# Performance work log

Measured on AMD Instinct MI355X. Metric: run time of the kernel, lower is better.

## Reference

```python
import jax, jax.numpy as jnp
import numpy as np

N = 50000      # nodes
E = 800000     # edges
IN_DIM = 256
HID = 96
OUT = 64
K = 2
ALPHA = 0.15
SCALING = 1.8  # NormalizedGCNConv scaling_factor
EPS = 1e-12    # torch F.normalize eps


def setup_inputs() -> dict:
    key = jax.random.key(0)
    ks = jax.random.split(key, 8)
    x = jax.random.normal(ks[0], (N, IN_DIM), jnp.float32)
    edge_index = jax.random.randint(ks[1], (2, E), 0, N, dtype=jnp.int64)
    def lin(k, fi, fo):
        s = 1.0 / np.sqrt(fi)
        kw, kb = jax.random.split(k)
        W = jax.random.uniform(kw, (fi, fo), jnp.float32, -s, s)
        b = jax.random.uniform(kb, (fo,), jnp.float32, -s, s)
        return W, b
    W0, b0 = lin(ks[2], IN_DIM, HID)   # convs[0]
    W1, b1 = lin(ks[3], HID, HID)      # convs[1]
    Wx, bx = lin(ks[4], HID, OUT)      # convx
    return {"x": x, "edge_index": edge_index,
            "W0": W0, "b0": b0, "W1": W1, "b1": b1, "Wx": Wx, "bx": bx}


def _l2norm(x):
    n = jnp.linalg.norm(x, axis=1, keepdims=True)
    return x / jnp.maximum(n, EPS)


def _gcn_norm(edge_index):
    # add self loops, symmetric normalization D^-1/2 (A+I) D^-1/2
    loop = jnp.arange(N, dtype=edge_index.dtype)
    row = jnp.concatenate([edge_index[0], loop])
    col = jnp.concatenate([edge_index[1], loop])
    deg = jax.ops.segment_sum(jnp.ones(row.shape[0], jnp.float32), col, num_segments=N)
    dinv = jnp.where(deg > 0, jax.lax.rsqrt(jnp.maximum(deg, 1.0)), 0.0)
    norm = dinv[row] * dinv[col]   # [E+N]
    return row, col, norm


def _norm_gcn_conv(x, W, b, row, col, norm):
    # linear -> L2 normalize * 1.8 -> APPNP(K, alpha), eval mode (no dropout)
    x = x @ W + b
    x = _l2norm(x) * SCALING
    h = x
    for _ in range(K):
        agg = jax.ops.segment_sum(x[row] * norm[:, None], col, num_segments=N)
        x = (1.0 - ALPHA) * agg + ALPHA * h
    return x


def reference(x, edge_index, W0, b0, W1, b1, Wx, bx):
    row, col, norm = _gcn_norm(edge_index)
    out = jax.nn.relu(_norm_gcn_conv(x, W0, b0, row, col, norm))
    # depth=3, link_len=2: loop runs i=1 only, residual condition never fires
    out = _l2norm(_norm_gcn_conv(out, W1, b1, row, col, norm)) * 1.5
    return _norm_gcn_conv(out, Wx, bx, row, col, norm)
```

## Files before the change

kernel.cpp:

```cpp
#include <hip/hip_runtime.h>
#include <hip/hip_fp16.h>
#include <math.h>

#define BETA_C 0.85f
#define ALF_C  0.15f
#define SLOTS 48
#define SCALE_Q 16.0f
#define INV_SQ  0.0625f

typedef _Float16 f16x8 __attribute__((ext_vector_type(8)));
typedef float f32x4 __attribute__((ext_vector_type(4)));
typedef float f32x2 __attribute__((ext_vector_type(2)));
typedef int i32x4 __attribute__((ext_vector_type(4)));

__device__ inline f16x8 as_h8(uint4 v) { union { uint4 u; f16x8 h; } U; U.u = v; return U.h; }

__device__ inline void unpack8(uint4 v, float* f) {
    union { uint4 u; _Float16 h[8]; } U; U.u = v;
#pragma unroll
    for (int i = 0; i < 8; ++i) f[i] = (float)U.h[i];
}

__device__ inline void acc_q(uint2 q, float* acc) {
    f32x2 f0 = __builtin_amdgcn_cvt_pk_f32_fp8((int)q.x, false);
    f32x2 f1 = __builtin_amdgcn_cvt_pk_f32_fp8((int)q.x, true);
    f32x2 f2 = __builtin_amdgcn_cvt_pk_f32_fp8((int)q.y, false);
    f32x2 f3 = __builtin_amdgcn_cvt_pk_f32_fp8((int)q.y, true);
    acc[0] += f0.x; acc[1] += f0.y; acc[2] += f1.x; acc[3] += f1.y;
    acc[4] += f2.x; acc[5] += f2.y; acc[6] += f3.x; acc[7] += f3.y;
}
__device__ inline uint2 pack_q(const float* r) {
    int lo = __builtin_amdgcn_cvt_pk_fp8_f32(r[0] * SCALE_Q, r[1] * SCALE_Q, 0, false);
    lo = __builtin_amdgcn_cvt_pk_fp8_f32(r[2] * SCALE_Q, r[3] * SCALE_Q, lo, true);
    int hi = __builtin_amdgcn_cvt_pk_fp8_f32(r[4] * SCALE_Q, r[5] * SCALE_Q, 0, false);
    hi = __builtin_amdgcn_cvt_pk_fp8_f32(r[6] * SCALE_Q, r[7] * SCALE_Q, hi, true);
    return make_uint2((unsigned)lo, (unsigned)hi);
}

__global__ __launch_bounds__(256) void k_fill_tlp(
        const int* __restrict__ row, const int* __restrict__ col,
        int* __restrict__ cur, int* __restrict__ adj, int E, unsigned mulc) {
    int cls = blockIdx.x & 7;
    int e = (blockIdx.x >> 3) * 256 + threadIdx.x;
    if (e >= E) return;
    int c = __builtin_nontemporal_load(col + e);
    if ((int)(((unsigned long long)(unsigned)c * mulc) >> 32) != cls) return;
    int r = __builtin_nontemporal_load(row + e);
    int p = atomicAdd(&cur[c], 1);
    if (p < SLOTS) adj[(size_t)c * SLOTS + p] = r;
}

__global__ void k_prep(const int* __restrict__ cur, float2* __restrict__ dinv2,
                       int* __restrict__ adj, int n, int t0,
                       const float* __restrict__ W0, const float* __restrict__ W1,
                       const float* __restrict__ Wx, ushort* __restrict__ WT0,
                       ushort* __restrict__ WT1, ushort* __restrict__ WTx) {
    int idx = blockIdx.x * blockDim.x + threadIdx.x;
    if (idx < n) {
        int deg = cur[idx];
        float degf = (float)deg + 1.0f;
        dinv2[idx] = make_float2(rsqrtf(degf), ALF_C * sqrtf(degf));
        int ds = min(deg, SLOTS);
        int d4 = (ds + 3) & ~3;
        int* ap = adj + (size_t)idx * SLOTS;
        for (int p = ds; p < d4; ++p) ap[p] = idx;
    } else if (idx >= t0) {
        const int S0 = 96 * 256, S1 = 96 * 96, S2 = 64 * 96;
        int li = idx - t0;
        const float* W; ushort* WT; int FI, FO;
        if (li < S0)           { W = W0; WT = WT0; FI = 256; FO = 96; }
        else if (li < S0 + S1) { W = W1; WT = WT1; FI = 96;  FO = 96; li -= S0; }
        else if (li < S0+S1+S2){ W = Wx; WT = WTx; FI = 96;  FO = 64; li -= S0 + S1; }
        else return;
        int nrow = li / FI, k = li % FI;
        _Float16 hv = (_Float16)W[(size_t)k * FO + nrow];
        WT[li] = *(ushort*)&hv;
    }
}

template<int FI, int FO, int ASRC_F16, int WQ>
__global__ __launch_bounds__(256) void k_gemm_mfma(
        const void* __restrict__ Xv, const ushort* __restrict__ WT,
        const float* __restrict__ Bias, const float2* __restrict__ dinv2,
        ushort* __restrict__ H, unsigned char* __restrict__ Hq,
        int n, float scale) {
    constexpr int NT = FO / 16;
    constexpr int CPR = FI / 8;
    __shared__ ushort sA[64 * FI];
    __shared__ ushort sW[FO * FI];
    const int tid = threadIdx.x;
    const int rb = blockIdx.x * 64;

    {
        constexpr int TOT = FO * CPR;
#pragma unroll
        for (int idx = tid; idx < TOT; idx += 256) {
            int nrow = idx / CPR, c = idx % CPR;
            uint4 v = *(((const uint4*)WT) + (size_t)nrow * CPR + c);
            int byte = ((nrow * FI + c * 8) * 2) ^ ((nrow & 7) << 4);
            *(uint4*)((char*)sW + byte) = v;
        }
    }
    {
        constexpr int TOT = 64 * CPR;
#pragma unroll
        for (int idx = tid; idx < TOT; idx += 256) {
            int r = idx / CPR, c = idx % CPR;
            int gr = rb + r;
            uint4 v = make_uint4(0u, 0u, 0u, 0u);
            if (ASRC_F16) {
                if (gr < n) v = *(((const uint4*)Xv) + (size_t)gr * CPR + c);
            } else {
                if (gr < n) {
                    const float4* Xp = (const float4*)Xv;
                    float4 f0 = Xp[(size_t)gr * (FI / 4) + c * 2];
                    float4 f1 = Xp[(size_t)gr * (FI / 4) + c * 2 + 1];
                    _Float16 hv[8] = {(_Float16)f0.x, (_Float16)f0.y, (_Float16)f0.z,
                                      (_Float16)f0.w, (_Float16)f1.x, (_Float16)f1.y,
                                      (_Float16)f1.z, (_Float16)f1.w};
                    v = *(uint4*)hv;
                }
            }
            int byte = ((r * FI + c * 8) * 2) ^ ((r & 7) << 4);
            *(uint4*)((char*)sA + byte) = v;
        }
    }
    __syncthreads();

    const int lane = tid & 63;
    const int wave = tid >> 6;
    const int lcol = lane & 15;
    const int lk = lane >> 4;

    f32x4 acc[NT];
#pragma unroll
    for (int t = 0; t < NT; ++t) acc[t] = (f32x4){0.f, 0.f, 0.f, 0.f};

    const int arow = wave * 16 + lcol;
    char* sAb = (char*)sA;
    char* sWb = (char*)sW;
#pragma unroll
    for (int s = 0; s < FI / 32; ++s) {
        int abyte = ((arow * FI + s * 32 + lk * 8) * 2) ^ ((arow & 7) << 4);
        f16x8 af = *(f16x8*)(sAb + abyte);
#pragma unroll
        for (int t = 0; t < NT; ++t) {
            int nrow = t * 16 + lcol;
            int bbyte = ((nrow * FI + s * 32 + lk * 8) * 2) ^ ((nrow & 7) << 4);
            f16x8 bf = *(f16x8*)(sWb + bbyte);
            acc[t] = __builtin_amdgcn_mfma_f32_16x16x32_f16(af, bf, acc[t], 0, 0, 0);
        }
    }

    float bv[NT];
#pragma unroll
    for (int t = 0; t < NT; ++t) bv[t] = Bias[t * 16 + lcol];
    float ss[4] = {0.f, 0.f, 0.f, 0.f};
#pragma unroll
    for (int t = 0; t < NT; ++t)
#pragma unroll
        for (int r = 0; r < 4; ++r) {
            acc[t][r] += bv[t];
            ss[r] += acc[t][r] * acc[t][r];
        }
    for (int m = 1; m < 16; m <<= 1) {
#pragma unroll
        for (int r = 0; r < 4; ++r) ss[r] += __shfl_xor(ss[r], m, 64);
    }
#pragma unroll
    for (int r = 0; r < 4; ++r) {
        int grow = rb + wave * 16 + lk * 4 + r;
        if (grow < n) {
            float sc = scale * dinv2[grow].x / fmaxf(sqrtf(ss[r]), 1e-12f);
#pragma unroll
            for (int t = 0; t < NT; ++t) {
                float v = acc[t][r] * sc;
                _Float16 hv = (_Float16)v;
                H[(size_t)grow * FO + t * 16 + lcol] = *(ushort*)&hv;
                if (WQ) {
                    float vs = v * SCALE_Q;
                    int b = __builtin_amdgcn_cvt_pk_fp8_f32(vs, vs, 0, false);
                    Hq[(size_t)grow * FO + t * 16 + lcol] = (unsigned char)(b & 0xff);
                }
            }
        }
    }
}

template<int C8>
__device__ inline void gather_q(const unsigned char* __restrict__ tq,
                                const int* __restrict__ ap,
                                int d4, int j, float* acc) {
    const size_t RB = C8 * 8;
    const int jb = j * 8;
    int e = 0;
    for (; e + 8 <= d4; e += 8) {
        i32x4 a0 = __builtin_nontemporal_load((const i32x4*)ap + (e >> 2));
        i32x4 a1 = __builtin_nontemporal_load((const i32x4*)ap + (e >> 2) + 1);
        uint2 q0 = *(const uint2*)(tq + (size_t)(unsigned)a0[0] * RB + jb);
        uint2 q1 = *(const uint2*)(tq + (size_t)(unsigned)a0[1] * RB + jb);
        uint2 q2 = *(const uint2*)(tq + (size_t)(unsigned)a0[2] * RB + jb);
        uint2 q3 = *(const uint2*)(tq + (size_t)(unsigned)a0[3] * RB + jb);
        uint2 q4 = *(const uint2*)(tq + (size_t)(unsigned)a1[0] * RB + jb);
        uint2 q5 = *(const uint2*)(tq + (size_t)(unsigned)a1[1] * RB + jb);
        uint2 q6 = *(const uint2*)(tq + (size_t)(unsigned)a1[2] * RB + jb);
        uint2 q7 = *(const uint2*)(tq + (size_t)(unsigned)a1[3] * RB + jb);
        acc_q(q0, acc); acc_q(q1, acc); acc_q(q2, acc); acc_q(q3, acc);
        acc_q(q4, acc); acc_q(q5, acc); acc_q(q6, acc); acc_q(q7, acc);
    }
    if (e < d4) {
        i32x4 a0 = __builtin_nontemporal_load((const i32x4*)ap + (e >> 2));
        uint2 q0 = *(const uint2*)(tq + (size_t)(unsigned)a0[0] * RB + jb);
        uint2 q1 = *(const uint2*)(tq + (size_t)(unsigned)a0[1] * RB + jb);
        uint2 q2 = *(const uint2*)(tq + (size_t)(unsigned)a0[2] * RB + jb);
        uint2 q3 = *(const uint2*)(tq + (size_t)(unsigned)a0[3] * RB + jb);
        acc_q(q0, acc); acc_q(q1, acc); acc_q(q2, acc); acc_q(q3, acc);
    }
}

template<int C8>
__device__ inline void gather_h(const uint4* __restrict__ tab,
                                const int* __restrict__ ap,
                                int d4, int j, f16x8& A0, f16x8& A1) {
    int e = 0;
    for (; e + 8 <= d4; e += 8) {
        i32x4 a0 = __builtin_nontemporal_load((const i32x4*)ap + (e >> 2));
        i32x4 a1 = __builtin_nontemporal_load((const i32x4*)ap + (e >> 2) + 1);
        uint4 v0 = tab[(size_t)(unsigned)a0[0] * C8 + j];
        uint4 v1 = tab[(size_t)(unsigned)a0[1] * C8 + j];
        uint4 v2 = tab[(size_t)(unsigned)a0[2] * C8 + j];
        uint4 v3 = tab[(size_t)(unsigned)a0[3] * C8 + j];
        uint4 v4 = tab[(size_t)(unsigned)a1[0] * C8 + j];
        uint4 v5 = tab[(size_t)(unsigned)a1[1] * C8 + j];
        uint4 v6 = tab[(size_t)(unsigned)a1[2] * C8 + j];
        uint4 v7 = tab[(size_t)(unsigned)a1[3] * C8 + j];
        A0 += (as_h8(v0) + as_h8(v1)) + (as_h8(v2) + as_h8(v3));
        A1 += (as_h8(v4) + as_h8(v5)) + (as_h8(v6) + as_h8(v7));
    }
    if (e < d4) {
        i32x4 a0 = __builtin_nontemporal_load((const i32x4*)ap + (e >> 2));
        uint4 v0 = tab[(size_t)(unsigned)a0[0] * C8 + j];
        uint4 v1 = tab[(size_t)(unsigned)a0[1] * C8 + j];
        uint4 v2 = tab[(size_t)(unsigned)a0[2] * C8 + j];
        uint4 v3 = tab[(size_t)(unsigned)a0[3] * C8 + j];
        A0 += as_h8(v0) + as_h8(v1);
        A1 += as_h8(v2) + as_h8(v3);
    }
}

template<int C8, int TPB, int QG, int WQ>
__global__ __launch_bounds__(TPB) void k_prop1(
        const uint4* __restrict__ y0h, const unsigned char* __restrict__ y0q,
        uint4* __restrict__ y1h, unsigned char* __restrict__ y1q,
        const int* __restrict__ adj, const int* __restrict__ cnt,
        const float2* __restrict__ dinv2, int n) {
    int tid = threadIdx.x;
    int j = tid % C8, cl = tid / C8;
    int c = blockIdx.x * (TPB / C8) + cl;
    if (c >= n) return;
    uint4 sv = y0h[(size_t)c * C8 + j];
    float d = dinv2[c].x;
    float a = BETA_C * d * d;
    int deg = min(cnt[c], SLOTS);
    int d4 = (deg + 3) & ~3;
    float coef_s = (a + ALF_C) - a * (float)(d4 - deg);
    float acc[8] = {0, 0, 0, 0, 0, 0, 0, 0};
    if (QG) {
        gather_q<C8>(y0q, adj + (size_t)c * SLOTS, d4, j, acc);
#pragma unroll
        for (int i = 0; i < 8; ++i) acc[i] *= INV_SQ;
    } else {
        f16x8 A0 = {0, 0, 0, 0, 0, 0, 0, 0};
        f16x8 A1 = {0, 0, 0, 0, 0, 0, 0, 0};
        gather_h<C8>(y0h, adj + (size_t)c * SLOTS, d4, j, A0, A1);
#pragma unroll
        for (int i = 0; i < 8; ++i) acc[i] = (float)A0[i] + (float)A1[i];
    }
    float sf[8];
    unpack8(sv, sf);
    float r[8];
    _Float16 hv[8];
#pragma unroll
    for (int i = 0; i < 8; ++i) {
        r[i] = a * acc[i] + coef_s * sf[i];
        hv[i] = (_Float16)r[i];
    }
    y1h[(size_t)c * C8 + j] = *(uint4*)hv;
    if (WQ) *(uint2*)(y1q + (size_t)c * (C8 * 8) + j * 8) = pack_q(r);
}

template<int C8, int TPB, int ACT, int OUTF32, int NORM, int QG>
__global__ __launch_bounds__(TPB) void k_prop2(
        const uint4* __restrict__ y1h, const unsigned char* __restrict__ y1q,
        const uint4* __restrict__ y0h, void* __restrict__ out,
        const int* __restrict__ adj, const int* __restrict__ cnt,
        const float2* __restrict__ dinv2, int n, float nscale) {
    __shared__ float ssh[NORM ? TPB : 1];
    int tid = threadIdx.x;
    int j = tid % C8, cl = tid / C8;
    int c = blockIdx.x * (TPB / C8) + cl;
    if (!NORM && c >= n) return;
    bool on = !NORM || c < n;
    float res[8] = {0, 0, 0, 0, 0, 0, 0, 0};
    if (on) {
        uint4 sv1 = y1h[(size_t)c * C8 + j];
        uint4 sv0 = y0h[(size_t)c * C8 + j];
        float2 dv = dinv2[c];
        float a = BETA_C * dv.x;
        float t = dv.y;
        int deg = min(cnt[c], SLOTS);
        int d4 = (deg + 3) & ~3;
        float coef_s = a * (1.0f - (float)(d4 - deg));
        float acc[8] = {0, 0, 0, 0, 0, 0, 0, 0};
        if (QG) {
            gather_q<C8>(y1q, adj + (size_t)c * SLOTS, d4, j, acc);
#pragma unroll
            for (int i = 0; i < 8; ++i) acc[i] *= INV_SQ;
        } else {
            f16x8 A0 = {0, 0, 0, 0, 0, 0, 0, 0};
            f16x8 A1 = {0, 0, 0, 0, 0, 0, 0, 0};
            gather_h<C8>(y1h, adj + (size_t)c * SLOTS, d4, j, A0, A1);
#pragma unroll
            for (int i = 0; i < 8; ++i) acc[i] = (float)A0[i] + (float)A1[i];
        }
        float sf[8], tf[8];
        unpack8(sv1, sf);
        unpack8(sv0, tf);
#pragma unroll
        for (int i = 0; i < 8; ++i) {
            res[i] = a * acc[i] + coef_s * sf[i] + t * tf[i];
            if (ACT) res[i] = fmaxf(res[i], 0.f);
        }
    }
    if (NORM) {
        float part = 0.f;
#pragma unroll
        for (int i = 0; i < 8; ++i) part += res[i] * res[i];
        ssh[tid] = part;
        __syncthreads();
        if (!on) return;
        float tot = 0.f;
#pragma unroll
        for (int q = 0; q < C8; ++q) tot += ssh[cl * C8 + q];
        float sc = nscale / fmaxf(sqrtf(tot), 1e-12f);
        _Float16 hv[8];
#pragma unroll
        for (int i = 0; i < 8; ++i) hv[i] = (_Float16)(res[i] * sc);
        ((uint4*)out)[(size_t)c * C8 + j] = *(uint4*)hv;
    } else if (OUTF32) {
        float4* op = (float4*)out;
        op[(size_t)c * (C8 * 2) + j * 2]     = make_float4(res[0], res[1], res[2], res[3]);
        op[(size_t)c * (C8 * 2) + j * 2 + 1] = make_float4(res[4], res[5], res[6], res[7]);
    } else {
        _Float16 hv[8];
#pragma unroll
        for (int i = 0; i < 8; ++i) hv[i] = (_Float16)res[i];
        ((uint4*)out)[(size_t)c * C8 + j] = *(uint4*)hv;
    }
}

extern "C" void kernel_launch(void* const* d_in, const int* in_sizes, int n_in,
                              void* d_out, int out_size, void* d_ws, size_t ws_size,
                              hipStream_t stream) {
    const float* x  = (const float*)d_in[0];
    const int*   ei = (const int*)d_in[1];
    const float* W0 = (const float*)d_in[2];
    const float* b0 = (const float*)d_in[3];
    const float* W1 = (const float*)d_in[4];
    const float* b1 = (const float*)d_in[5];
    const float* Wx = (const float*)d_in[6];
    const float* bx = (const float*)d_in[7];
    float* out = (float*)d_out;

    const int N = in_sizes[0] / 256;
    const int E = in_sizes[1] / 2;
    const int* row = ei;
    const int* col = ei + E;

    char* ws = (char*)d_ws;
    size_t off = 0;
    auto alloc = [&](size_t bytes) -> char* {
        char* p = ws + off;
        off += (bytes + 255) & ~(size_t)255;
        return p;
    };
    int*    cur   = (int*)alloc((size_t)N * 4);
    float2* dinv2 = (float2*)alloc((size_t)N * 8);
    int*    adj   = (int*)alloc((size_t)N * SLOTS * 4);
    ushort* WT0   = (ushort*)alloc((size_t)96 * 256 * 2);
    ushort* WT1   = (ushort*)alloc((size_t)96 * 96 * 2);
    ushort* WTx   = (ushort*)alloc((size_t)64 * 96 * 2);
    ushort* Hh    = (ushort*)alloc((size_t)N * 96 * 2);
    ushort* T1h   = (ushort*)alloc((size_t)N * 96 * 2);
    ushort* T2h   = (ushort*)alloc((size_t)N * 96 * 2);
    unsigned char* Hq  = (unsigned char*)alloc((size_t)N * 96);
    unsigned char* T1q = (unsigned char*)alloc((size_t)N * 96);
    (void)ws_size; (void)n_in; (void)out_size;

    unsigned mulc = (unsigned)((((unsigned long long)8 << 32) + (unsigned)N - 1) / (unsigned)N);

    hipMemsetAsync(cur, 0, (size_t)N * 4, stream);
    {
        int chunks = (E + 255) / 256;
        k_fill_tlp<<<chunks * 8, 256, 0, stream>>>(row, col, cur, adj, E, mulc);
    }
    {
        int t0 = ((N + 255) / 256) * 256;
        int tot = t0 + 96 * 256 + 96 * 96 + 64 * 96;
        k_prep<<<(tot + 255) / 256, 256, 0, stream>>>(cur, dinv2, adj, N, t0,
                                                      W0, W1, Wx, WT0, WT1, WTx);
    }

    int gblk = (N + 63) / 64;
    int gp12 = (N + 15) / 16;
    int gp8  = (N + 31) / 32;

    k_gemm_mfma<256, 96, 0, 1><<<gblk, 256, 0, stream>>>(x, WT0, b0, dinv2, Hh, Hq, N, 1.8f);
    k_prop1<12, 192, 1, 1><<<gp12, 192, 0, stream>>>(
        (const uint4*)Hh, Hq, (uint4*)T1h, T1q, adj, cur, dinv2, N);
    k_prop2<12, 192, 1, 0, 0, 1><<<gp12, 192, 0, stream>>>(
        (const uint4*)T1h, T1q, (const uint4*)Hh, T2h, adj, cur, dinv2, N, 0.f);

    k_gemm_mfma<96, 96, 1, 1><<<gblk, 256, 0, stream>>>(T2h, WT1, b1, dinv2, Hh, Hq, N, 1.8f);
    k_prop1<12, 192, 1, 1><<<gp12, 192, 0, stream>>>(
        (const uint4*)Hh, Hq, (uint4*)T1h, T1q, adj, cur, dinv2, N);
    k_prop2<12, 192, 0, 0, 1, 1><<<gp12, 192, 0, stream>>>(
        (const uint4*)T1h, T1q, (const uint4*)Hh, T2h, adj, cur, dinv2, N, 1.5f);

    k_gemm_mfma<96, 64, 1, 0><<<gblk, 256, 0, stream>>>(T2h, WTx, bx, dinv2, Hh, Hq, N, 1.8f);
    k_prop1<8, 256, 0, 0><<<gp8, 256, 0, stream>>>(
        (const uint4*)Hh, Hq, (uint4*)T1h, T1q, adj, cur, dinv2, N);
    k_prop2<8, 256, 0, 1, 0, 0><<<gp8, 256, 0, stream>>>(
        (const uint4*)T1h, T1q, (const uint4*)Hh, out, adj, cur, dinv2, N, 0.f);
}
```

Measured before the change: 216.0 us.

## Widen propagation gathers to 16 fp8 per lane and vectorize edge fill

Propagation kernels now have each thread handle 16 features, gathering 16-byte fp8 rows instead of 8-byte chunks. This halves the threads per node and doubles bytes per load. The last layer also switches from fp16 gathers to fp8-quantized gathers, adding quantization error to the final output. The fill kernel reads edges four at a time with vector loads, which cuts index traffic and the number of threads.

Result: slower. 221.0 us (+2.3%).

```diff
diff --git a/kernel.cpp b/kernel.cpp
--- a/kernel.cpp
+++ b/kernel.cpp
@@ -29,6 +29,10 @@
     acc[0] += f0.x; acc[1] += f0.y; acc[2] += f1.x; acc[3] += f1.y;
     acc[4] += f2.x; acc[5] += f2.y; acc[6] += f3.x; acc[7] += f3.y;
 }
+__device__ inline void acc16(uint4 q, float* acc) {
+    acc_q(make_uint2(q.x, q.y), acc);
+    acc_q(make_uint2(q.z, q.w), acc + 8);
+}
 __device__ inline uint2 pack_q(const float* r) {
     int lo = __builtin_amdgcn_cvt_pk_fp8_f32(r[0] * SCALE_Q, r[1] * SCALE_Q, 0, false);
     lo = __builtin_amdgcn_cvt_pk_fp8_f32(r[2] * SCALE_Q, r[3] * SCALE_Q, lo, true);
@@ -37,17 +41,45 @@
     return make_uint2((unsigned)lo, (unsigned)hi);
 }
 
-__global__ __launch_bounds__(256) void k_fill_tlp(
+__global__ __launch_bounds__(256) void k_fill_q(
         const int* __restrict__ row, const int* __restrict__ col,
         int* __restrict__ cur, int* __restrict__ adj, int E, unsigned mulc) {
     int cls = blockIdx.x & 7;
-    int e = (blockIdx.x >> 3) * 256 + threadIdx.x;
+    int q = (blockIdx.x >> 3) * 256 + threadIdx.x;
+    int e = q * 4;
     if (e >= E) return;
-    int c = __builtin_nontemporal_load(col + e);
-    if ((int)(((unsigned long long)(unsigned)c * mulc) >> 32) != cls) return;
-    int r = __builtin_nontemporal_load(row + e);
-    int p = atomicAdd(&cur[c], 1);
-    if (p < SLOTS) adj[(size_t)c * SLOTS + p] = r;
+    i32x4 cv;
+    bool full = (e + 3 < E);
+    if (full) {
+        cv = __builtin_nontemporal_load((const i32x4*)col + q);
+    } else {
+#pragma unroll
+        for (int i = 0; i < 4; ++i) cv[i] = (e + i < E) ? col[e + i] : 0;
+    }
+    bool m[4]; bool any = false;
+#pragma unroll
+    for (int i = 0; i < 4; ++i) {
+        bool valid = full || (e + i < E);
+        m[i] = valid &&
+               ((int)(((unsigned long long)(unsigned)cv[i] * mulc) >> 32) == cls);
+        any |= m[i];
+    }
+    if (!any) return;
+    i32x4 rv;
+    if (full) {
+        rv = __builtin_nontemporal_load((const i32x4*)row + q);
+    } else {
+#pragma unroll
+        for (int i = 0; i < 4; ++i) rv[i] = (e + i < E) ? row[e + i] : 0;
+    }
+#pragma unroll
+    for (int i = 0; i < 4; ++i) {
+        if (m[i]) {
+            int c = cv[i];
+            int p = atomicAdd(&cur[c], 1);
+            if (p < SLOTS) adj[(size_t)c * SLOTS + p] = rv[i];
+        }
+    }
 }
 
 __global__ void k_prep(const int* __restrict__ cur, float2* __restrict__ dinv2,
@@ -78,7 +110,7 @@
     }
 }
 
-template<int FI, int FO, int ASRC_F16, int WQ>
+template<int FI, int FO, int ASRC_F16>
 __global__ __launch_bounds__(256) void k_gemm_mfma(
         const void* __restrict__ Xv, const ushort* __restrict__ WT,
         const float* __restrict__ Bias, const float2* __restrict__ dinv2,
@@ -177,185 +209,155 @@
                 float v = acc[t][r] * sc;
                 _Float16 hv = (_Float16)v;
                 H[(size_t)grow * FO + t * 16 + lcol] = *(ushort*)&hv;
-                if (WQ) {
-                    float vs = v * SCALE_Q;
-                    int b = __builtin_amdgcn_cvt_pk_fp8_f32(vs, vs, 0, false);
-                    Hq[(size_t)grow * FO + t * 16 + lcol] = (unsigned char)(b & 0xff);
-                }
+                float vs = v * SCALE_Q;
+                int b = __builtin_amdgcn_cvt_pk_fp8_f32(vs, vs, 0, false);
+                Hq[(size_t)grow * FO + t * 16 + lcol] = (unsigned char)(b & 0xff);
             }
         }
     }
 }
 
-template<int C8>
-__device__ inline void gather_q(const unsigned char* __restrict__ tq,
-                                const int* __restrict__ ap,
-                                int d4, int j, float* acc) {
-    const size_t RB = C8 * 8;
-    const int jb = j * 8;
+template<int RB>
+__device__ inline void gather_q16(const unsigned char* __restrict__ tq,
+                                  const int* __restrict__ ap,
+                                  int d4, int jb, float* acc) {
     int e = 0;
     for (; e + 8 <= d4; e += 8) {
         i32x4 a0 = __builtin_nontemporal_load((const i32x4*)ap + (e >> 2));
         i32x4 a1 = __builtin_nontemporal_load((const i32x4*)ap + (e >> 2) + 1);
-        uint2 q0 = *(const uint2*)(tq + (size_t)(unsigned)a0[0] * RB + jb);
-        uint2 q1 = *(const uint2*)(tq + (size_t)(unsigned)a0[1] * RB + jb);
-        uint2 q2 = *(const uint2*)(tq + (size_t)(unsigned)a0[2] * RB + jb);
-        uint2 q3 = *(const uint2*)(tq + (size_t)(unsigned)a0[3] * RB + jb);
-        uint2 q4 = *(const uint2*)(tq + (size_t)(unsigned)a1[0] * RB + jb);
-        uint2 q5 = *(const uint2*)(tq + (size_t)(unsigned)a1[1] * RB + jb);
-        uint2 q6 = *(const uint2*)(tq + (size_t)(unsigned)a1[2] * RB + jb);
-        uint2 q7 = *(const uint2*)(tq + (size_t)(unsigned)a1[3] * RB + jb);
-        acc_q(q0, acc); acc_q(q1, acc); acc_q(q2, acc); acc_q(q3, acc);
-        acc_q(q4, acc); acc_q(q5, acc); acc_q(q6, acc); acc_q(q7, acc);
+        uint4 v0 = *(const uint4*)(tq + (size_t)(unsigned)a0[0] * RB + jb);
+        uint4 v1 = *(const uint4*)(tq + (size_t)(unsigned)a0[1] * RB + jb);
+        uint4 v2 = *(const uint4*)(tq + (size_t)(unsigned)a0[2] * RB + jb);
+        uint4 v3 = *(const uint4*)(tq + (size_t)(unsigned)a0[3] * RB + jb);
+        uint4 v4 = *(const uint4*)(tq + (size_t)(unsigned)a1[0] * RB + jb);
+        uint4 v5 = *(const uint4*)(tq + (size_t)(unsigned)a1[1] * RB + jb);
+        uint4 v6 = *(const uint4*)(tq + (size_t)(unsigned)a1[2] * RB + jb);
+        uint4 v7 = *(const uint4*)(tq + (size_t)(unsigned)a1[3] * RB + jb);
+        acc16(v0, acc); acc16(v1, acc); acc16(v2, acc); acc16(v3, acc);
+        acc16(v4, acc); acc16(v5, acc); acc16(v6, acc); acc16(v7, acc);
     }
     if (e < d4) {
         i32x4 a0 = __builtin_nontemporal_load((const i32x4*)ap + (e >> 2));
-        uint2 q0 = *(const uint2*)(tq + (size_t)(unsigned)a0[0] * RB + jb);
-        uint2 q1 = *(const uint2*)(tq + (size_t)(unsigned)a0[1] * RB + jb);
-        uint2 q2 = *(const uint2*)(tq + (size_t)(unsigned)a0[2] * RB + jb);
-        uint2 q3 = *(const uint2*)(tq + (size_t)(unsigned)a0[3] * RB + jb);
-        acc_q(q0, acc); acc_q(q1, acc); acc_q(q2, acc); acc_q(q3, acc);
-    }
-}
-
-template<int C8>
-__device__ inline void gather_h(const uint4* __restrict__ tab,
-                                const int* __restrict__ ap,
-                                int d4, int j, f16x8& A0, f16x8& A1) {
-    int e = 0;
-    for (; e + 8 <= d4; e += 8) {
-        i32x4 a0 = __builtin_nontemporal_load((const i32x4*)ap + (e >> 2));
-        i32x4 a1 = __builtin_nontemporal_load((const i32x4*)ap + (e >> 2) + 1);
-        uint4 v0 = tab[(size_t)(unsigned)a0[0] * C8 + j];
-        uint4 v1 = tab[(size_t)(unsigned)a0[1] * C8 + j];
-        uint4 v2 = tab[(size_t)(unsigned)a0[2] * C8 + j];
-        uint4 v3 = tab[(size_t)(unsigned)a0[3] * C8 + j];
-        uint4 v4 = tab[(size_t)(unsigned)a1[0] * C8 + j];
-        uint4 v5 = tab[(size_t)(unsigned)a1[1] * C8 + j];
-        uint4 v6 = tab[(size_t)(unsigned)a1[2] * C8 + j];
-        uint4 v7 = tab[(size_t)(unsigned)a1[3] * C8 + j];
-        A0 += (as_h8(v0) + as_h8(v1)) + (as_h8(v2) + as_h8(v3));
-        A1 += (as_h8(v4) + as_h8(v5)) + (as_h8(v6) + as_h8(v7));
-    }
-    if (e < d4) {
-        i32x4 a0 = __builtin_nontemporal_load((const i32x4*)ap + (e >> 2));
-        uint4 v0 = tab[(size_t)(unsigned)a0[0] * C8 + j];
-        uint4 v1 = tab[(size_t)(unsigned)a0[1] * C8 + j];
-        uint4 v2 = tab[(size_t)(unsigned)a0[2] * C8 + j];
-        uint4 v3 = tab[(size_t)(unsigned)a0[3] * C8 + j];
-        A0 += as_h8(v0) + as_h8(v1);
-        A1 += as_h8(v2) + as_h8(v3);
-    }
-}
-
-template<int C8, int TPB, int QG, int WQ>
-__global__ __launch_bounds__(TPB) void k_prop1(
+        uint4 v0 = *(const uint4*)(tq + (size_t)(unsigned)a0[0] * RB + jb);
+        uint4 v1 = *(const uint4*)(tq + (size_t)(unsigned)a0[1] * RB + jb);
+        uint4 v2 = *(const uint4*)(tq + (size_t)(unsigned)a0[2] * RB + jb);
+        uint4 v3 = *(const uint4*)(tq + (size_t)(unsigned)a0[3] * RB + jb);
+        acc16(v0, acc); acc16(v1, acc); acc16(v2, acc); acc16(v3, acc);
+    }
+}
+
+template<int CQ, int TPB>
+__global__ __launch_bounds__(TPB) void k_prop1_q(
         const uint4* __restrict__ y0h, const unsigned char* __restrict__ y0q,
         uint4* __restrict__ y1h, unsigned char* __restrict__ y1q,
         const int* __restrict__ adj, const int* __restrict__ cnt,
         const float2* __restrict__ dinv2, int n) {
+    constexpr int C8H = CQ * 2;
+    constexpr int RB = CQ * 16;
     int tid = threadIdx.x;
-    int j = tid % C8, cl = tid / C8;
-    int c = blockIdx.x * (TPB / C8) + cl;
+    int j = tid % CQ, cl = tid / CQ;
+    int c = blockIdx.x * (TPB / CQ) + cl;
     if (c >= n) return;
-    uint4 sv = y0h[(size_t)c * C8 + j];
+    uint4 sv0 = y0h[(size_t)c * C8H + j * 2];
+    uint4 sv1 = y0h[(size_t)c * C8H + j * 2 + 1];
     float d = dinv2[c].x;
     float a = BETA_C * d * d;
     int deg = min(cnt[c], SLOTS);
     int d4 = (deg + 3) & ~3;
     float coef_s = (a + ALF_C) - a * (float)(d4 - deg);
-    float acc[8] = {0, 0, 0, 0, 0, 0, 0, 0};
-    if (QG) {
-        gather_q<C8>(y0q, adj + (size_t)c * SLOTS, d4, j, acc);
-#pragma unroll
-        for (int i = 0; i < 8; ++i) acc[i] *= INV_SQ;
-    } else {
-        f16x8 A0 = {0, 0, 0, 0, 0, 0, 0, 0};
-        f16x8 A1 = {0, 0, 0, 0, 0, 0, 0, 0};
-        gather_h<C8>(y0h, adj + (size_t)c * SLOTS, d4, j, A0, A1);
-#pragma unroll
-        for (int i = 0; i < 8; ++i) acc[i] = (float)A0[i] + (float)A1[i];
-    }
-    float sf[8];
-    unpack8(sv, sf);
-    float r[8];
-    _Float16 hv[8];
-#pragma unroll
-    for (int i = 0; i < 8; ++i) {
-        r[i] = a * acc[i] + coef_s * sf[i];
+    float aq = a * INV_SQ;
+    float acc[16];
+#pragma unroll
+    for (int i = 0; i < 16; ++i) acc[i] = 0.f;
+    gather_q16<RB>(y0q, adj + (size_t)c * SLOTS, d4, j * 16, acc);
+    float sf[16];
+    unpack8(sv0, sf);
+    unpack8(sv1, sf + 8);
+    float r[16];
+    _Float16 hv[16];
+#pragma unroll
+    for (int i = 0; i < 16; ++i) {
+        r[i] = aq * acc[i] + coef_s * sf[i];
         hv[i] = (_Float16)r[i];
     }
-    y1h[(size_t)c * C8 + j] = *(uint4*)hv;
-    if (WQ) *(uint2*)(y1q + (size_t)c * (C8 * 8) + j * 8) = pack_q(r);
-}
-
-template<int C8, int TPB, int ACT, int OUTF32, int NORM, int QG>
-__global__ __launch_bounds__(TPB) void k_prop2(
+    y1h[(size_t)c * C8H + j * 2]     = ((uint4*)hv)[0];
+    y1h[(size_t)c * C8H + j * 2 + 1] = ((uint4*)hv)[1];
+    uint2 qlo = pack_q(r);
+    uint2 qhi = pack_q(r + 8);
+    *(uint4*)(y1q + (size_t)c * RB + j * 16) = make_uint4(qlo.x, qlo.y, qhi.x, qhi.y);
+}
+
+template<int CQ, int TPB, int ACT, int OUTF32, int NORM>
+__global__ __launch_bounds__(TPB) void k_prop2_q(
         const uint4* __restrict__ y1h, const unsigned char* __restrict__ y1q,
         const uint4* __restrict__ y0h, void* __restrict__ out,
         const int* __restrict__ adj, const int* __restrict__ cnt,
         const float2* __restrict__ dinv2, int n, float nscale) {
+    constexpr int C8H = CQ * 2;
+    constexpr int RB = CQ * 16;
     __shared__ float ssh[NORM ? TPB : 1];
     int tid = threadIdx.x;
-    int j = tid % C8, cl = tid / C8;
-    int c = blockIdx.x * (TPB / C8) + cl;
+    int j = tid % CQ, cl = tid / CQ;
+    int c = blockIdx.x * (TPB / CQ) + cl;
     if (!NORM && c >= n) return;
     bool on = !NORM || c < n;
-    float res[8] = {0, 0, 0, 0, 0, 0, 0, 0};
+    float res[16];
+#pragma unroll
+    for (int i = 0; i < 16; ++i) res[i] = 0.f;
     if (on) {
-        uint4 sv1 = y1h[(size_t)c * C8 + j];
-        uint4 sv0 = y0h[(size_t)c * C8 + j];
+        uint4 sva = y1h[(size_t)c * C8H + j * 2];
+        uint4 svb = y1h[(size_t)c * C8H + j * 2 + 1];
+        uint4 tva = y0h[(size_t)c * C8H + j * 2];
+        uint4 tvb = y0h[(size_t)c * C8H + j * 2 + 1];
         float2 dv = dinv2[c];
         float a = BETA_C * dv.x;
         float t = dv.y;
         int deg = min(cnt[c], SLOTS);
         int d4 = (deg + 3) & ~3;
         float coef_s = a * (1.0f - (float)(d4 - deg));
-        float acc[8] = {0, 0, 0, 0, 0, 0, 0, 0};
-        if (QG) {
-            gather_q<C8>(y1q, adj + (size_t)c * SLOTS, d4, j, acc);
-#pragma unroll
-            for (int i = 0; i < 8; ++i) acc[i] *= INV_SQ;
-        } else {
-            f16x8 A0 = {0, 0, 0, 0, 0, 0, 0, 0};
-            f16x8 A1 = {0, 0, 0, 0, 0, 0, 0, 0};
-            gather_h<C8>(y1h, adj + (size_t)c * SLOTS, d4, j, A0, A1);
-#pragma unroll
-            for (int i = 0; i < 8; ++i) acc[i] = (float)A0[i] + (float)A1[i];
-        }
-        float sf[8], tf[8];
-        unpack8(sv1, sf);
-        unpack8(sv0, tf);
-#pragma unroll
-        for (int i = 0; i < 8; ++i) {
-            res[i] = a * acc[i] + coef_s * sf[i] + t * tf[i];
+        float aq = a * INV_SQ;
+        float acc[16];
+#pragma unroll
+        for (int i = 0; i < 16; ++i) acc[i] = 0.f;
+        gather_q16<RB>(y1q, adj + (size_t)c * SLOTS, d4, j * 16, acc);
+        float sf[16], tf[16];
+        unpack8(sva, sf); unpack8(svb, sf + 8);
+        unpack8(tva, tf); unpack8(tvb, tf + 8);
+#pragma unroll
+        for (int i = 0; i < 16; ++i) {
+            res[i] = aq * acc[i] + coef_s * sf[i] + t * tf[i];
             if (ACT) res[i] = fmaxf(res[i], 0.f);
         }
     }
     if (NORM) {
         float part = 0.f;
 #pragma unroll
-        for (int i = 0; i < 8; ++i) part += res[i] * res[i];
+        for (int i = 0; i < 16; ++i) part += res[i] * res[i];
         ssh[tid] = part;
         __syncthreads();
         if (!on) return;
         float tot = 0.f;
 #pragma unroll
-        for (int q = 0; q < C8; ++q) tot += ssh[cl * C8 + q];
+        for (int q = 0; q < CQ; ++q) tot += ssh[cl * CQ + q];
         float sc = nscale / fmaxf(sqrtf(tot), 1e-12f);
-        _Float16 hv[8];
-#pragma unroll
-        for (int i = 0; i < 8; ++i) hv[i] = (_Float16)(res[i] * sc);
-        ((uint4*)out)[(size_t)c * C8 + j] = *(uint4*)hv;
+        _Float16 hv[16];
+#pragma unroll
+        for (int i = 0; i < 16; ++i) hv[i] = (_Float16)(res[i] * sc);
+        ((uint4*)out)[(size_t)c * C8H + j * 2]     = ((uint4*)hv)[0];
+        ((uint4*)out)[(size_t)c * C8H + j * 2 + 1] = ((uint4*)hv)[1];
     } else if (OUTF32) {
         float4* op = (float4*)out;
-        op[(size_t)c * (C8 * 2) + j * 2]     = make_float4(res[0], res[1], res[2], res[3]);
-        op[(size_t)c * (C8 * 2) + j * 2 + 1] = make_float4(res[4], res[5], res[6], res[7]);
+        size_t base = (size_t)c * (CQ * 4) + j * 4;
+#pragma unroll
+        for (int k = 0; k < 4; ++k)
+            op[base + k] = make_float4(res[k * 4], res[k * 4 + 1],
+                                       res[k * 4 + 2], res[k * 4 + 3]);
     } else {
-        _Float16 hv[8];
-#pragma unroll
-        for (int i = 0; i < 8; ++i) hv[i] = (_Float16)res[i];
-        ((uint4*)out)[(size_t)c * C8 + j] = *(uint4*)hv;
+        _Float16 hv[16];
+#pragma unroll
+        for (int i = 0; i < 16; ++i) hv[i] = (_Float16)res[i];
+        ((uint4*)out)[(size_t)c * C8H + j * 2]     = ((uint4*)hv)[0];
+        ((uint4*)out)[(size_t)c * C8H + j * 2 + 1] = ((uint4*)hv)[1];
     }
 }
 
@@ -401,8 +403,9 @@
 
     hipMemsetAsync(cur, 0, (size_t)N * 4, stream);
     {
-        int chunks = (E + 255) / 256;
-        k_fill_tlp<<<chunks * 8, 256, 0, stream>>>(row, col, cur, adj, E, mulc);
+        int quads = (E + 3) / 4;
+        int chunks = (quads + 255) / 256;
+        k_fill_q<<<chunks * 8, 256, 0, stream>>>(row, col, cur, adj, E, mulc);
     }
     {
         int t0 = ((N + 255) / 256) * 256;
@@ -412,24 +415,24 @@
     }
 
     int gblk = (N + 63) / 64;
-    int gp12 = (N + 15) / 16;
-    int gp8  = (N + 31) / 32;
-
-    k_gemm_mfma<256, 96, 0, 1><<<gblk, 256, 0, stream>>>(x, WT0, b0, dinv2, Hh, Hq, N, 1.8f);
-    k_prop1<12, 192, 1, 1><<<gp12, 192, 0, stream>>>(
+    int gp96 = (N + 31) / 32;
+    int gp64 = (N + 63) / 64;
+
+    k_gemm_mfma<256, 96, 0><<<gblk, 256, 0, stream>>>(x, WT0, b0, dinv2, Hh, Hq, N, 1.8f);
+    k_prop1_q<6, 192><<<gp96, 192, 0, stream>>>(
         (const uint4*)Hh, Hq, (uint4*)T1h, T1q, adj, cur, dinv2, N);
-    k_prop2<12, 192, 1, 0, 0, 1><<<gp12, 192, 0, stream>>>(
+    k_prop2_q<6, 192, 1, 0, 0><<<gp96, 192, 0, stream>>>(
         (const uint4*)T1h, T1q, (const uint4*)Hh, T2h, adj, cur, dinv2, N, 0.f);
 
-    k_gemm_mfma<96, 96, 1, 1><<<gblk, 256, 0, stream>>>(T2h, WT1, b1, dinv2, Hh, Hq, N, 1.8f);
-    k_prop1<12, 192, 1, 1><<<gp12, 192, 0, stream>>>(
+    k_gemm_mfma<96, 96, 1><<<gblk, 256, 0, stream>>>(T2h, WT1, b1, dinv2, Hh, Hq, N, 1.8f);
+    k_prop1_q<6, 192><<<gp96, 192, 0, stream>>>(
         (const uint4*)Hh, Hq, (uint4*)T1h, T1q, adj, cur, dinv2, N);
-    k_prop2<12, 192, 0, 0, 1, 1><<<gp12, 192, 0, stream>>>(
+    k_prop2_q<6, 192, 0, 0, 1><<<gp96, 192, 0, stream>>>(
         (const uint4*)T1h, T1q, (const uint4*)Hh, T2h, adj, cur, dinv2, N, 1.5f);
 
-    k_gemm_mfma<96, 64, 1, 0><<<gblk, 256, 0, stream>>>(T2h, WTx, bx, dinv2, Hh, Hq, N, 1.8f);
-    k_prop1<8, 256, 0, 0><<<gp8, 256, 0, stream>>>(
+    k_gemm_mfma<96, 64, 1><<<gblk, 256, 0, stream>>>(T2h, WTx, bx, dinv2, Hh, Hq, N, 1.8f);
+    k_prop1_q<4, 256><<<gp64, 256, 0, stream>>>(
         (const uint4*)Hh, Hq, (uint4*)T1h, T1q, adj, cur, dinv2, N);
-    k_prop2<8, 256, 0, 1, 0, 0><<<gp8, 256, 0, stream>>>(
+    k_prop2_q<4, 256, 0, 1, 0><<<gp64, 256, 0, stream>>>(
         (const uint4*)T1h, T1q, (const uint4*)Hh, out, adj, cur, dinv2, N, 0.f);
 }
```
